# Kernel optimization log

Measured on AMD Instinct MI355X. Metric: run time of the kernel, lower is better.

## Reference

```python
import jax, jax.numpy as jnp
import numpy as np

DIM = 192
WS = (7, 7, 7)
NUM_HEADS = 6
N = WS[0] * WS[1] * WS[2]  # 343
HEAD_DIM = DIM // NUM_HEADS
SCALE = HEAD_DIM ** -0.5
TABLE_SIZE = (2 * WS[0] - 1) * (2 * WS[1] - 1) * (2 * WS[2] - 1)  # 2197


def _relative_position_index():
    coords = np.stack(np.meshgrid(np.arange(WS[0]), np.arange(WS[1]), np.arange(WS[2])))
    cf = coords.reshape(3, -1)  # [3, N]
    rel = cf[:, :, None] - cf[:, None, :]  # [3, N, N]
    rel = rel.transpose(1, 2, 0)
    rel[:, :, 0] += WS[0] - 1
    rel[:, :, 1] += WS[1] - 1
    rel[:, :, 2] += WS[2] - 1
    rel[:, :, 0] *= (2 * WS[1] - 1) * (2 * WS[2] - 1)
    rel[:, :, 1] *= 2 * WS[2] - 1
    return rel.sum(-1)  # [N, N] int


_RPI = jnp.asarray(_relative_position_index())


def setup_inputs() -> dict:
    key = jax.random.key(0)
    ks = jax.random.split(key, 6)
    B = 256
    x = jax.random.normal(ks[0], (B, N, DIM), dtype=jnp.float32)
    mask = jax.random.normal(ks[1], (64, N, N), dtype=jnp.float32)
    qkv_w = jax.random.normal(ks[2], (DIM, 3 * DIM), dtype=jnp.float32) * (DIM ** -0.5)
    rpb_table = jax.random.normal(ks[3], (TABLE_SIZE, NUM_HEADS), dtype=jnp.float32) * 0.02
    proj_w = jax.random.normal(ks[4], (DIM, DIM), dtype=jnp.float32) * (DIM ** -0.5)
    proj_b = jax.random.normal(ks[5], (DIM,), dtype=jnp.float32) * 0.01
    return {"x": x, "mask": mask, "qkv_w": qkv_w, "rpb_table": rpb_table,
            "proj_w": proj_w, "proj_b": proj_b}


def reference(x, mask, qkv_w, rpb_table, proj_w, proj_b):
    b, n, c = x.shape
    h = NUM_HEADS
    # qkv projection (no bias), split into q,k,v of shape [b, h, n, hd]
    qkv = (x @ qkv_w).reshape(b, n, 3, h, c // h).transpose(2, 0, 3, 1, 4)
    q, k, v = qkv[0], qkv[1], qkv[2]
    q = q * SCALE
    attn = jnp.einsum('bhqd,bhkd->bhqk', q, k)  # [b, h, n, n]
    # gathered relative position bias: [n, n, h] -> [h, n, n]
    bias = rpb_table[_RPI[:n, :n].reshape(-1)].reshape(n, n, h)
    attn = attn + jnp.transpose(bias, (2, 0, 1))[None]
    nw = mask.shape[0]
    nwww = max(b // nw, 1)
    attn = attn.reshape(nwww, nw, h, n, n) + mask[None, :, None]
    attn = attn.reshape(-1, h, n, n)
    attn = jax.nn.softmax(attn, axis=-1)
    out = jnp.einsum('bhqk,bhkd->bhqd', attn, v)
    out = jnp.swapaxes(out, 1, 2).reshape(b, n, c)
    return out @ proj_w + proj_b
```

## Files before the change

kernel.cpp:

```cpp
#include <hip/hip_runtime.h>

typedef __attribute__((ext_vector_type(8))) short bf16x8;
typedef __attribute__((ext_vector_type(4))) float f32x4;
typedef __attribute__((ext_vector_type(4))) int i32x4;

#define MFMA16(a,b,c) __builtin_amdgcn_mfma_f32_16x16x32_bf16(a,b,c,0,0,0)

#define SCALE 0.1767766952966369f

static __device__ __forceinline__ f32x4 zero4(){
    f32x4 z = {0.f,0.f,0.f,0.f};
    return z;
}
static __device__ __forceinline__ float bf2f(unsigned short u){
    unsigned int x = ((unsigned int)u) << 16;
    return __builtin_bit_cast(float, x);
}
static __device__ __forceinline__ unsigned short f2bf(float f){
    __bf16 b = (__bf16)f;
    return __builtin_bit_cast(unsigned short, b);
}
static __device__ __forceinline__ void bar_lds(){
    asm volatile("s_waitcnt lgkmcnt(0)" ::: "memory");
    __builtin_amdgcn_s_barrier();
}

__global__ __launch_bounds__(256) void k_prep_wt(const float* __restrict__ qkv_w,
                                                 unsigned short* __restrict__ wt){
    int i = blockIdx.x*256 + threadIdx.x;
    if (i < 576*192){ int n = i/192, kk = i%192; wt[i] = f2bf(qkv_w[kk*576 + n]); }
}
__global__ __launch_bounds__(256) void k_prep_pwt(const float* __restrict__ proj_w,
                                                  unsigned short* __restrict__ pwt){
    int i = blockIdx.x*256 + threadIdx.x;
    if (i < 192*192){ int n = i/192, kk = i%192; pwt[i] = f2bf(proj_w[kk*192 + n]); }
}
__global__ __launch_bounds__(256) void k_prep_bias(const float* __restrict__ rpb,
                                                   unsigned short* __restrict__ bias){
    int i = blockIdx.x*256 + threadIdx.x;
    if (i >= 6*343*352) return;
    int h = i / (343*352); int rem = i % (343*352);
    int qi = rem / 352, ci = rem % 352;
    unsigned short v = 0;
    if (ci < 343){
        int qa=qi/49, qr=qi%49, qb=qr/7, qc=qr%7;
        int ka=ci/49, kr=ci%49, kb=kr/7, kc=kr%7;
        int idx = 169*(qb-kb+6) + 13*(qa-ka+6) + (qc-kc+6);
        v = f2bf(rpb[idx*6 + h]);
    }
    bias[i] = v;
}

__global__ __launch_bounds__(256, 3) void k_qkv(const float* __restrict__ x,
                                                const unsigned short* __restrict__ wt,
                                                unsigned short* __restrict__ q,
                                                unsigned short* __restrict__ k,
                                                unsigned short* __restrict__ v){
    __shared__ __attribute__((aligned(16))) unsigned short Bs[2][192*40];
    const int tid = threadIdx.x;
    const int wid = tid>>6, lane = tid&63, quad = lane>>4, l15 = lane&15;
    const int nq = blockIdx.x % 3;
    const int mg = blockIdx.x / 3;
    const int srr = tid>>2, scc = (tid&3)<<3;

    f32x4 acc[24];
    #pragma unroll
    for (int i=0;i<24;++i) acc[i] = zero4();

    const unsigned short* wtb = wt + nq*192*192;
    i32x4 s0, s1, s2;
    s0 = *(const i32x4*)(wtb + (srr      )*192 + scc);
    s1 = *(const i32x4*)(wtb + (srr +  64)*192 + scc);
    s2 = *(const i32x4*)(wtb + (srr + 128)*192 + scc);

    const int r0 = mg*128 + wid*32 + l15;
    const float* xp0 = x + (long)r0*192 + quad*8;
    const float* xp1 = xp0 + 16*192;
    f32x4 xa0 = *(const f32x4*)(xp0);
    f32x4 xa1 = *(const f32x4*)(xp0+4);
    f32x4 xb0 = *(const f32x4*)(xp1);
    f32x4 xb1 = *(const f32x4*)(xp1+4);

    for (int k0=0; k0<6; ++k0){
        unsigned short* B = &Bs[k0&1][0];
        *(i32x4*)&B[(srr      )*40 + scc] = s0;
        *(i32x4*)&B[(srr +  64)*40 + scc] = s1;
        *(i32x4*)&B[(srr + 128)*40 + scc] = s2;
        if (k0 < 5){
            const unsigned short* wn = wtb + (k0+1)*32;
            s0 = *(const i32x4*)(wn + (srr      )*192 + scc);
            s1 = *(const i32x4*)(wn + (srr +  64)*192 + scc);
            s2 = *(const i32x4*)(wn + (srr + 128)*192 + scc);
        }
        bf16x8 a0, a1;
        #pragma unroll
        for (int j=0;j<4;++j){
            a0[j] = (short)f2bf(xa0[j]); a0[4+j] = (short)f2bf(xa1[j]);
            a1[j] = (short)f2bf(xb0[j]); a1[4+j] = (short)f2bf(xb1[j]);
        }
        if (k0 < 5){
            xa0 = *(const f32x4*)(xp0 + (k0+1)*32);
            xa1 = *(const f32x4*)(xp0 + (k0+1)*32 + 4);
            xb0 = *(const f32x4*)(xp1 + (k0+1)*32);
            xb1 = *(const f32x4*)(xp1 + (k0+1)*32 + 4);
        }
        bar_lds();
        #pragma unroll
        for (int nt=0; nt<12; ++nt){
            bf16x8 b = *(const bf16x8*)&B[(nt*16+l15)*40 + quad*8];
            acc[nt]    = MFMA16(a0, b, acc[nt]);
            acc[12+nt] = MFMA16(a1, b, acc[12+nt]);
        }
    }

    unsigned short* dst = (nq==0) ? q : (nq==1) ? k : v;
    const float mul = (nq==0) ? SCALE : 1.0f;
    #pragma unroll
    for (int mt=0; mt<2; ++mt){
        #pragma unroll
        for (int r=0; r<4; ++r){
            int tm = mg*128 + wid*32 + mt*16 + quad*4 + r;
            int bb = tm/343, tt = tm%343;
            #pragma unroll
            for (int nt=0; nt<12; ++nt){
                int cc = nt*16 + l15;
                int h = cc>>5, d = cc&31;
                dst[((bb*6+h)*343 + tt)*32 + d] = f2bf(acc[mt*12+nt][r]*mul);
            }
        }
    }
}

__global__ __launch_bounds__(256) void k_attn(const unsigned short* __restrict__ q,
                                              const unsigned short* __restrict__ kg,
                                              const unsigned short* __restrict__ vg,
                                              const float* __restrict__ mask,
                                              const unsigned short* __restrict__ bias,
                                              unsigned short* __restrict__ ao){
    __shared__ __attribute__((aligned(16))) unsigned short Ks[352*40];
    __shared__ __attribute__((aligned(16))) unsigned short Vs[32*344 + 64];
    __shared__ __attribute__((aligned(16))) unsigned short Pb[4*2*640];
    const int tid = threadIdx.x;
    const int wid = tid>>6, lane = tid&63, quad = lane>>4, l15 = lane&15;
    const int idx = blockIdx.x;
    const int w = idx/24, sub = idx%24, g = sub/6, h = sub%6, b = g*64 + w;
    const int bh = b*6 + h;
    const unsigned short* kb  = kg + bh*10976;
    const unsigned short* vb  = vg + bh*10976;
    const unsigned short* qb  = q  + bh*10976;
    const float*          mw  = mask + w*117649;
    const unsigned short* bhp = bias + h*120736;

    for (int i=tid; i<1372; i+=256){
        int rr=i>>2, cc=(i&3)<<3;
        *(i32x4*)&Ks[rr*40+cc] = *(const i32x4*)(kb + rr*32 + cc);
    }
    for (int i=tid; i<1372; i+=256){
        int tok=i>>2, c=(i&3)<<3;
        bf16x8 vv = *(const bf16x8*)(vb + tok*32 + c);
        #pragma unroll
        for (int j=0;j<8;++j) Vs[(c+j)*344 + tok] = (unsigned short)vv[j];
    }
    if (tid < 32) Vs[tid*344 + 343] = 0;
    if (tid < 64) Vs[32*344 + tid] = 0;
    __syncthreads();

    for (int chunk=wid; chunk<22; chunk+=4){
        int qrow = chunk*16 + l15; if (qrow > 342) qrow = 342;
        bf16x8 a = *(const bf16x8*)(qb + qrow*32 + quad*8);
        f32x4 s[22];
        #pragma unroll
        for (int t=0; t<22; ++t){
            bf16x8 bb = *(const bf16x8*)&Ks[(t*16+l15)*40 + quad*8];
            s[t] = MFMA16(a, bb, zero4());
        }
        const int row0 = chunk*16 + quad*4;
        #pragma unroll
        for (int r=0; r<4; ++r){
            int row = row0 + r; int rowc = row>342 ? 342 : row;
            const float*          mrow = mw  + rowc*343;
            const unsigned short* brow = bhp + rowc*352;
            #pragma unroll
            for (int t=0; t<22; ++t){
                int col  = t*16 + l15;
                int colc = col>342 ? 342 : col;
                s[t][r] += mrow[colc] + bf2f(brow[col]);
            }
        }
        if (l15 >= 7){
            #pragma unroll
            for (int r=0; r<4; ++r) s[21][r] = -1e30f;
        }
        f32x4 mx, sm, inv;
        #pragma unroll
        for (int r=0; r<4; ++r){
            float m = s[0][r];
            #pragma unroll
            for (int t=1; t<22; ++t) m = fmaxf(m, s[t][r]);
            mx[r] = m;
        }
        #pragma unroll
        for (int d=1; d<16; d<<=1){
            #pragma unroll
            for (int r=0; r<4; ++r) mx[r] = fmaxf(mx[r], __shfl_xor(mx[r], d));
        }
        #pragma unroll
        for (int r=0; r<4; ++r){
            float acc = 0.f;
            #pragma unroll
            for (int t=0; t<22; ++t){ float e = __expf(s[t][r]-mx[r]); s[t][r]=e; acc += e; }
            sm[r] = acc;
        }
        #pragma unroll
        for (int d=1; d<16; d<<=1){
            #pragma unroll
            for (int r=0; r<4; ++r) sm[r] += __shfl_xor(sm[r], d);
        }
        #pragma unroll
        for (int r=0; r<4; ++r) inv[r] = 1.0f / sm[r];

        f32x4 o0 = zero4(), o1 = zero4();
        unsigned short* pw0 = Pb + wid*1280;
        #pragma unroll
        for (int ks=0; ks<11; ++ks){
            unsigned short* pw = pw0 + (ks&1)*640;
            #pragma unroll
            for (int tt=0; tt<2; ++tt){
                int t = ks*2+tt;
                #pragma unroll
                for (int r=0; r<4; ++r)
                    pw[(quad*4+r)*40 + tt*16 + l15] = f2bf(s[t][r]*inv[r]);
            }
            asm volatile("s_waitcnt lgkmcnt(0)" ::: "memory");
            bf16x8 ap = *(const bf16x8*)&pw[l15*40 + quad*8];
            bf16x8 v0 = *(const bf16x8*)&Vs[l15*344      + ks*32 + quad*8];
            bf16x8 v1 = *(const bf16x8*)&Vs[(16+l15)*344 + ks*32 + quad*8];
            o0 = MFMA16(ap, v0, o0);
            o1 = MFMA16(ap, v1, o1);
        }
        #pragma unroll
        for (int r=0; r<4; ++r){
            int nt = row0 + r;
            if (nt < 343){
                unsigned short* dst = ao + (b*343 + nt)*192 + h*32;
                dst[l15]    = f2bf(o0[r]);
                dst[16+l15] = f2bf(o1[r]);
            }
        }
    }
}

__global__ __launch_bounds__(256) void k_proj(const unsigned short* __restrict__ ao,
                                              const unsigned short* __restrict__ pwt,
                                              const float* __restrict__ pbias,
                                              float* __restrict__ out){
    const int tid = threadIdx.x, wid = tid>>6, lane = tid&63, quad = lane>>4, l15 = lane&15;
    const int m0 = blockIdx.x*64 + wid*16;
    f32x4 acc[12];
    #pragma unroll
    for (int st=0; st<12; ++st) acc[st] = zero4();
    float bl[12];
    #pragma unroll
    for (int st=0; st<12; ++st) bl[st] = pbias[st*16 + l15];
    const unsigned short* arow = ao + (m0 + l15)*192 + quad*8;
    for (int k0=0; k0<192; k0+=32){
        bf16x8 a = *(const bf16x8*)(arow + k0);
        #pragma unroll
        for (int st=0; st<12; ++st){
            bf16x8 bb = *(const bf16x8*)(pwt + (st*16+l15)*192 + k0 + quad*8);
            acc[st] = MFMA16(a, bb, acc[st]);
        }
    }
    #pragma unroll
    for (int r=0; r<4; ++r){
        int tm = m0 + quad*4 + r;
        #pragma unroll
        for (int st=0; st<12; ++st)
            out[tm*192 + st*16 + l15] = acc[st][r] + bl[st];
    }
}

extern "C" void kernel_launch(void* const* d_in, const int* in_sizes, int n_in,
                              void* d_out, int out_size, void* d_ws, size_t ws_size,
                              hipStream_t stream){
    const float* x     = (const float*)d_in[0];
    const float* mask  = (const float*)d_in[1];
    const float* qkv_w = (const float*)d_in[2];
    const float* rpb   = (const float*)d_in[3];
    const float* projw = (const float*)d_in[4];
    const float* projb = (const float*)d_in[5];
    float* out = (float*)d_out;
    unsigned short* ws  = (unsigned short*)d_ws;

    unsigned short* wt   = ws;
    unsigned short* pwt  = wt   + 110592;
    unsigned short* bias = pwt  + 36864;
    unsigned short* q    = bias + 724416;
    unsigned short* k    = q    + 16859136;
    unsigned short* v    = k    + 16859136;
    unsigned short* ao   = v    + 16859136;

    hipLaunchKernelGGL(k_prep_wt,   dim3(432),  dim3(256), 0, stream, qkv_w, wt);
    hipLaunchKernelGGL(k_prep_pwt,  dim3(144),  dim3(256), 0, stream, projw, pwt);
    hipLaunchKernelGGL(k_prep_bias, dim3(2830), dim3(256), 0, stream, rpb, bias);
    hipLaunchKernelGGL(k_qkv,       dim3(2058), dim3(256), 0, stream, x, wt, q, k, v);
    hipLaunchKernelGGL(k_attn,      dim3(1536), dim3(256), 0, stream, q, k, v, mask, bias, ao);
    hipLaunchKernelGGL(k_proj,      dim3(1372), dim3(256), 0, stream, ao, pwt, projb, out);
}
```

Measured before the change: 459.5 us.

## Repad attention LDS strides, single-buffer P, stage proj weights in LDS

The attention kernel changes its K and V shared-memory padding strides, presumably to cut LDS bank conflicts. It also drops the double-buffered P tile to shrink LDS, and adds a launch_bounds occupancy hint of 3 blocks. The projection kernel now stages the full weight matrix in padded LDS, software-prefetches the next A fragment, and declares a 2-block occupancy hint. The trade-off is a 75 KB LDS footprint per projection block, which may limit occupancy. Single-buffering P could also add a write-after-read hazard between iterations.

```diff
diff --git a/kernel.cpp b/kernel.cpp
--- a/kernel.cpp
+++ b/kernel.cpp
@@ -7,6 +7,8 @@
 #define MFMA16(a,b,c) __builtin_amdgcn_mfma_f32_16x16x32_bf16(a,b,c,0,0,0)
 
 #define SCALE 0.1767766952966369f
+#define KP 36
+#define VP 346
 
 static __device__ __forceinline__ f32x4 zero4(){
     f32x4 z = {0.f,0.f,0.f,0.f};
@@ -131,15 +133,15 @@
     }
 }
 
-__global__ __launch_bounds__(256) void k_attn(const unsigned short* __restrict__ q,
+__global__ __launch_bounds__(256, 3) void k_attn(const unsigned short* __restrict__ q,
                                               const unsigned short* __restrict__ kg,
                                               const unsigned short* __restrict__ vg,
                                               const float* __restrict__ mask,
                                               const unsigned short* __restrict__ bias,
                                               unsigned short* __restrict__ ao){
-    __shared__ __attribute__((aligned(16))) unsigned short Ks[352*40];
-    __shared__ __attribute__((aligned(16))) unsigned short Vs[32*344 + 64];
-    __shared__ __attribute__((aligned(16))) unsigned short Pb[4*2*640];
+    __shared__ __attribute__((aligned(16))) unsigned short Ks[352*KP];
+    __shared__ __attribute__((aligned(16))) unsigned short Vs[32*VP + 64];
+    __shared__ __attribute__((aligned(16))) unsigned short Pb[4*640];
     const int tid = threadIdx.x;
     const int wid = tid>>6, lane = tid&63, quad = lane>>4, l15 = lane&15;
     const int idx = blockIdx.x;
@@ -153,16 +155,18 @@
 
     for (int i=tid; i<1372; i+=256){
         int rr=i>>2, cc=(i&3)<<3;
-        *(i32x4*)&Ks[rr*40+cc] = *(const i32x4*)(kb + rr*32 + cc);
+        *(i32x4*)&Ks[rr*KP+cc] = *(const i32x4*)(kb + rr*32 + cc);
     }
     for (int i=tid; i<1372; i+=256){
         int tok=i>>2, c=(i&3)<<3;
         bf16x8 vv = *(const bf16x8*)(vb + tok*32 + c);
         #pragma unroll
-        for (int j=0;j<8;++j) Vs[(c+j)*344 + tok] = (unsigned short)vv[j];
-    }
-    if (tid < 32) Vs[tid*344 + 343] = 0;
-    if (tid < 64) Vs[32*344 + tid] = 0;
+        for (int j=0;j<8;++j) Vs[(c+j)*VP + tok] = (unsigned short)vv[j];
+    }
+    if (tid < 32){
+        Vs[tid*VP + 343] = 0; Vs[tid*VP + 344] = 0; Vs[tid*VP + 345] = 0;
+    }
+    if (tid < 64) Vs[32*VP + tid] = 0;
     __syncthreads();
 
     for (int chunk=wid; chunk<22; chunk+=4){
@@ -171,7 +175,7 @@
         f32x4 s[22];
         #pragma unroll
         for (int t=0; t<22; ++t){
-            bf16x8 bb = *(const bf16x8*)&Ks[(t*16+l15)*40 + quad*8];
+            bf16x8 bb = *(const bf16x8*)&Ks[(t*16+l15)*KP + quad*8];
             s[t] = MFMA16(a, bb, zero4());
         }
         const int row0 = chunk*16 + quad*4;
@@ -220,10 +224,9 @@
         for (int r=0; r<4; ++r) inv[r] = 1.0f / sm[r];
 
         f32x4 o0 = zero4(), o1 = zero4();
-        unsigned short* pw0 = Pb + wid*1280;
+        unsigned short* pw = Pb + wid*640;
         #pragma unroll
         for (int ks=0; ks<11; ++ks){
-            unsigned short* pw = pw0 + (ks&1)*640;
             #pragma unroll
             for (int tt=0; tt<2; ++tt){
                 int t = ks*2+tt;
@@ -233,8 +236,8 @@
             }
             asm volatile("s_waitcnt lgkmcnt(0)" ::: "memory");
             bf16x8 ap = *(const bf16x8*)&pw[l15*40 + quad*8];
-            bf16x8 v0 = *(const bf16x8*)&Vs[l15*344      + ks*32 + quad*8];
-            bf16x8 v1 = *(const bf16x8*)&Vs[(16+l15)*344 + ks*32 + quad*8];
+            bf16x8 v0 = *(const bf16x8*)&Vs[l15*VP      + ks*32 + quad*8];
+            bf16x8 v1 = *(const bf16x8*)&Vs[(16+l15)*VP + ks*32 + quad*8];
             o0 = MFMA16(ap, v0, o0);
             o1 = MFMA16(ap, v1, o1);
         }
@@ -250,12 +253,19 @@
     }
 }
 
-__global__ __launch_bounds__(256) void k_proj(const unsigned short* __restrict__ ao,
+__global__ __launch_bounds__(256, 2) void k_proj(const unsigned short* __restrict__ ao,
                                               const unsigned short* __restrict__ pwt,
                                               const float* __restrict__ pbias,
                                               float* __restrict__ out){
+    __shared__ __attribute__((aligned(16))) unsigned short Ws[192*200];
     const int tid = threadIdx.x, wid = tid>>6, lane = tid&63, quad = lane>>4, l15 = lane&15;
     const int m0 = blockIdx.x*64 + wid*16;
+
+    for (int i=tid; i<4608; i+=256){
+        int rr = i/24, cc = (i%24)<<3;
+        *(i32x4*)&Ws[rr*200+cc] = *(const i32x4*)(pwt + rr*192 + cc);
+    }
+
     f32x4 acc[12];
     #pragma unroll
     for (int st=0; st<12; ++st) acc[st] = zero4();
@@ -263,13 +273,18 @@
     #pragma unroll
     for (int st=0; st<12; ++st) bl[st] = pbias[st*16 + l15];
     const unsigned short* arow = ao + (m0 + l15)*192 + quad*8;
-    for (int k0=0; k0<192; k0+=32){
-        bf16x8 a = *(const bf16x8*)(arow + k0);
+    bf16x8 a = *(const bf16x8*)(arow);
+    __syncthreads();
+
+    for (int k0=0; k0<6; ++k0){
+        bf16x8 an;
+        if (k0 < 5) an = *(const bf16x8*)(arow + (k0+1)*32);
         #pragma unroll
         for (int st=0; st<12; ++st){
-            bf16x8 bb = *(const bf16x8*)(pwt + (st*16+l15)*192 + k0 + quad*8);
+            bf16x8 bb = *(const bf16x8*)&Ws[(st*16+l15)*200 + k0*32 + quad*8];
             acc[st] = MFMA16(a, bb, acc[st]);
         }
+        a = an;
     }
     #pragma unroll
     for (int r=0; r<4; ++r){
```

After: 714.9 us. 55.6% more time.
